# Optimization experiments

Hardware: AMD Instinct MI355X
Metric: run time of the kernel (lower is better)

## Reference

```python
import jax, jax.numpy as jnp
import numpy as np

N_NODES = 100000
N_EDGES = 1600000
IN_DIM = 64
HID = 128
N_GRAPHS = 64
N_CLASSES = 2
EPS = 1e-5


def setup_inputs() -> dict:
    key = jax.random.key(0)
    ks = jax.random.split(key, 8)
    x = jax.random.normal(ks[0], (N_NODES, IN_DIM), dtype=jnp.float32)
    edge_index = jax.random.randint(ks[1], (2, N_EDGES), 0, N_NODES, dtype=jnp.int64)
    batch = jnp.sort(jax.random.randint(ks[2], (N_NODES,), 0, N_GRAPHS, dtype=jnp.int64))
    W1 = jax.random.normal(ks[3], (IN_DIM, HID), dtype=jnp.float32) / np.sqrt(IN_DIM)
    b1 = jnp.zeros((HID,), jnp.float32)
    W2 = jax.random.normal(ks[4], (HID, HID), dtype=jnp.float32) / np.sqrt(HID)
    b2 = jnp.zeros((HID,), jnp.float32)
    gamma = jnp.ones((HID,), jnp.float32)
    beta = jnp.zeros((HID,), jnp.float32)
    fcW = jax.random.normal(ks[5], (HID, N_CLASSES), dtype=jnp.float32) / np.sqrt(HID)
    fcb = jnp.zeros((N_CLASSES,), jnp.float32)
    return {"x": x, "edge_index": edge_index, "batch": batch, "W1": W1, "b1": b1,
            "W2": W2, "b2": b2, "gamma": gamma, "beta": beta, "fcW": fcW, "fcb": fcb}


def reference(x, edge_index, batch, W1, b1, W2, b2, gamma, beta, fcW, fcb):
    n = x.shape[0]
    loop = jnp.arange(n)
    # GCNConv adds self-loops and uses symmetric normalization D^-1/2 (A+I) D^-1/2
    src = jnp.concatenate([edge_index[0], loop])
    dst = jnp.concatenate([edge_index[1], loop])
    deg = jax.ops.segment_sum(jnp.ones_like(dst, dtype=x.dtype), dst, num_segments=n)
    dis = jax.lax.rsqrt(deg)  # deg >= 1 thanks to self-loops
    enorm = dis[src] * dis[dst]  # [E+N]

    def gcn(h, W, b):
        h = h @ W                                   # transform first (PyG order)
        msg = h[src] * enorm[:, None]               # gather + scale
        return jax.ops.segment_sum(msg, dst, num_segments=n) + b  # scatter-add

    cnt = jnp.maximum(jax.ops.segment_sum(jnp.ones((n,), x.dtype), batch,
                                          num_segments=N_GRAPHS), 1.0)[:, None]

    def inst_norm(h):
        # per-graph, per-channel normalization over nodes (affine=False)
        mean = jax.ops.segment_sum(h, batch, num_segments=N_GRAPHS) / cnt
        var = jax.ops.segment_sum(h * h, batch, num_segments=N_GRAPHS) / cnt - mean * mean
        return (h - mean[batch]) * jax.lax.rsqrt(var[batch] + EPS)

    h = jax.nn.relu(inst_norm(gcn(x, W1, b1)))   # dropout = identity (eval)
    h = jax.nn.relu(inst_norm(gcn(h, W2, b2)))
    pooled = jax.ops.segment_sum(h, batch, num_segments=N_GRAPHS) / cnt  # global mean pool
    # BatchNorm1d over the graph dimension (batch statistics, affine)
    m = jnp.mean(pooled, axis=0)
    v = jnp.mean((pooled - m) ** 2, axis=0)
    z = (pooled - m) * jax.lax.rsqrt(v + EPS) * gamma + beta
    return z @ fcW + fcb
```

## Files before the change

kernel.cpp:

```cpp
#include <hip/hip_runtime.h>
#include <hip/hip_bf16.h>


#define HID 128
#define NGRAPH 64
#define EPSN 1e-5f
#define BSHIFT 8
#define NBMAX 512
#define REP 4
#define NH (NGRAPH * HID)

typedef unsigned int uint;
typedef unsigned short ushort;
typedef __attribute__((ext_vector_type(8))) short short8;
typedef __attribute__((ext_vector_type(4))) float f32x4;

static __device__ __forceinline__ ushort f2bf(float f) {
  uint x = __float_as_uint(f);
  return (ushort)((x + 0x7FFFu + ((x >> 16) & 1u)) >> 16);
}
static __device__ __forceinline__ uint pack2(float a, float b) {
  return (uint)f2bf(a) | ((uint)f2bf(b) << 16);
}
static __device__ __forceinline__ float bf_lo(uint u) { return __uint_as_float(u << 16); }
static __device__ __forceinline__ float bf_hi(uint u) {
  return __uint_as_float(u & 0xFFFF0000u);
}

__global__ __launch_bounds__(256) void graph_starts(const int* __restrict__ batch,
                                                    int* __restrict__ gstart, int N) {
  int i = blockIdx.x * 256 + threadIdx.x;
  if (i >= N) return;
  int g = batch[i];
  if (i == 0) {
    for (int q = 0; q <= g; ++q) gstart[q] = 0;
  } else {
    int gp = batch[i - 1];
    if (g != gp)
      for (int q = gp + 1; q <= g; ++q) gstart[q] = i;
  }
  if (i == N - 1)
    for (int q = g + 1; q <= NGRAPH; ++q) gstart[q] = N;
}

__global__ __launch_bounds__(256) void bin_edges(const int* __restrict__ src,
                                                 const int* __restrict__ dst,
                                                 int* __restrict__ gcursor,
                                                 uint* __restrict__ records, int E, int NB,
                                                 int cap) {
  __shared__ int h[NBMAX];
  __shared__ int base[NBMAX];
  for (int i = threadIdx.x; i < NB; i += 256) h[i] = 0;
  __syncthreads();
  int e0 = blockIdx.x * 4096;
  int d[16], s[16];
#pragma unroll
  for (int k = 0; k < 16; ++k) {
    int e = e0 + k * 256 + threadIdx.x;
    if (e < E) {
      d[k] = dst[e];
      s[k] = src[e];
      atomicAdd(&h[d[k] >> BSHIFT], 1);
    }
  }
  __syncthreads();
  for (int i = threadIdx.x; i < NB; i += 256) {
    int c = h[i];
    if (c) base[i] = i * cap + atomicAdd(&gcursor[i], c);
  }
  __syncthreads();
  for (int i = threadIdx.x; i < NB; i += 256) h[i] = 0;
  __syncthreads();
#pragma unroll
  for (int k = 0; k < 16; ++k) {
    int e = e0 + k * 256 + threadIdx.x;
    if (e < E) {
      int b = d[k] >> BSHIFT;
      int lp = atomicAdd(&h[b], 1);
      records[base[b] + lp] = ((uint)s[k] << 8) | (uint)(d[k] & 255);
    }
  }
}

__global__ __launch_bounds__(256) void build_csr(const uint* __restrict__ records,
                                                 const int* __restrict__ gcursor,
                                                 int* __restrict__ row_beg,
                                                 int* __restrict__ row_end,
                                                 float* __restrict__ dis,
                                                 int* __restrict__ esrc, int N, int cap) {
  const int b = blockIdx.x;
  const int node0 = b << BSHIFT;
  const int nn = min(256, N - node0);
  const int beg = b * cap;
  const int cnt = gcursor[b];
  const int t = threadIdx.x;
  __shared__ int lc[256], sc[256], lcur[256];
  lc[t] = 0;
  __syncthreads();
  for (int i = t; i < cnt; i += 256) atomicAdd(&lc[records[beg + i] & 255u], 1);
  __syncthreads();
  int myc = lc[t];
  sc[t] = myc;
  __syncthreads();
  for (int off = 1; off < 256; off <<= 1) {
    int add = (t >= off) ? sc[t - off] : 0;
    __syncthreads();
    sc[t] += add;
    __syncthreads();
  }
  int excl = sc[t] - myc;
  if (t < nn) {
    row_beg[node0 + t] = beg + excl;
    row_end[node0 + t] = beg + excl + myc;
    dis[node0 + t] = rsqrtf((float)myc + 1.0f);
  }
  lcur[t] = excl;
  __syncthreads();
  for (int i = t; i < cnt; i += 256) {
    uint r = records[beg + i];
    int p = atomicAdd(&lcur[r & 255u], 1);
    esrc[beg + p] = (int)(r >> 8);
  }
}

__global__ __launch_bounds__(256) void xscale_bf16(const float* __restrict__ X,
                                                   const float* __restrict__ dis,
                                                   ushort* __restrict__ XS, int n4) {
  int i4 = blockIdx.x * 256 + threadIdx.x;
  if (i4 >= n4) return;
  int n = i4 >> 4;
  float dn = dis[n];
  float4 v = ((const float4*)X)[i4];
  ushort4 u;
  u.x = f2bf(v.x * dn);
  u.y = f2bf(v.y * dn);
  u.z = f2bf(v.z * dn);
  u.w = f2bf(v.w * dn);
  ((ushort4*)XS)[i4] = u;
}

__global__ __launch_bounds__(256) void wt_both(const float* __restrict__ W1,
                                               const float* __restrict__ W2,
                                               ushort* __restrict__ w1t,
                                               ushort* __restrict__ w2t) {
  int i = blockIdx.x * 256 + threadIdx.x;
  if (i < 128 * 64) {
    int c = i / 64, k = i - c * 64;
    w1t[i] = f2bf(W1[(size_t)k * HID + c]);
  } else {
    int i2 = i - 128 * 64;
    if (i2 < 128 * 128) {
      int c = i2 / 128, k = i2 - c * 128;
      w2t[i2] = f2bf(W2[(size_t)k * HID + c]);
    }
  }
}

__global__ __launch_bounds__(256) void aggregate64(const ushort* __restrict__ XS,
                                                   const int* __restrict__ row_beg,
                                                   const int* __restrict__ row_end,
                                                   const int* __restrict__ esrc,
                                                   const float* __restrict__ dis,
                                                   ushort* __restrict__ out, int N) {
  int wave = (int)((blockIdx.x * 256 + threadIdx.x) >> 6);
  const int l = threadIdx.x & 63;
  const int n = wave * 4 + (l >> 4);
  if (n >= N) return;
  const int j = l & 15;
  const float dn = dis[n];
  const int beg = row_beg[n];
  const int len = row_end[n] - beg;
  const uint2* Xj = (const uint2*)XS + j;
  float a0 = 0.f, a1 = 0.f, a2 = 0.f, a3 = 0.f;
  float b0 = 0.f, b1 = 0.f, b2 = 0.f, b3 = 0.f;
  int i = 0;
  for (; i + 7 < len; i += 8) {
    int s0 = esrc[beg + i], s1 = esrc[beg + i + 1];
    int s2 = esrc[beg + i + 2], s3 = esrc[beg + i + 3];
    int s4 = esrc[beg + i + 4], s5 = esrc[beg + i + 5];
    int s6 = esrc[beg + i + 6], s7 = esrc[beg + i + 7];
    uint2 u0 = Xj[(size_t)s0 * 16];
    uint2 u1 = Xj[(size_t)s1 * 16];
    uint2 u2 = Xj[(size_t)s2 * 16];
    uint2 u3 = Xj[(size_t)s3 * 16];
    uint2 u4 = Xj[(size_t)s4 * 16];
    uint2 u5 = Xj[(size_t)s5 * 16];
    uint2 u6 = Xj[(size_t)s6 * 16];
    uint2 u7 = Xj[(size_t)s7 * 16];
    a0 += bf_lo(u0.x) + bf_lo(u1.x) + bf_lo(u2.x) + bf_lo(u3.x);
    a1 += bf_hi(u0.x) + bf_hi(u1.x) + bf_hi(u2.x) + bf_hi(u3.x);
    a2 += bf_lo(u0.y) + bf_lo(u1.y) + bf_lo(u2.y) + bf_lo(u3.y);
    a3 += bf_hi(u0.y) + bf_hi(u1.y) + bf_hi(u2.y) + bf_hi(u3.y);
    b0 += bf_lo(u4.x) + bf_lo(u5.x) + bf_lo(u6.x) + bf_lo(u7.x);
    b1 += bf_hi(u4.x) + bf_hi(u5.x) + bf_hi(u6.x) + bf_hi(u7.x);
    b2 += bf_lo(u4.y) + bf_lo(u5.y) + bf_lo(u6.y) + bf_lo(u7.y);
    b3 += bf_hi(u4.y) + bf_hi(u5.y) + bf_hi(u6.y) + bf_hi(u7.y);
  }
  for (; i < len; ++i) {
    uint2 u = Xj[(size_t)esrc[beg + i] * 16];
    a0 += bf_lo(u.x);
    a1 += bf_hi(u.x);
    a2 += bf_lo(u.y);
    a3 += bf_hi(u.y);
  }
  uint2 us = Xj[(size_t)n * 16];
  a0 += b0 + bf_lo(us.x);
  a1 += b1 + bf_hi(us.x);
  a2 += b2 + bf_lo(us.y);
  a3 += b3 + bf_hi(us.y);
  uint2 o;
  o.x = pack2(a0 * dn, a1 * dn);
  o.y = pack2(a2 * dn, a3 * dn);
  ((uint2*)out)[(size_t)n * 16 + j] = o;
}

__global__ __launch_bounds__(256) void aggregate128(const ushort* __restrict__ H,
                                                    const int* __restrict__ row_beg,
                                                    const int* __restrict__ row_end,
                                                    const int* __restrict__ esrc,
                                                    const float* __restrict__ dis,
                                                    const float* __restrict__ bias,
                                                    ushort* __restrict__ outz, int N) {
  int wave = (int)((blockIdx.x * 256 + threadIdx.x) >> 6);
  const int l = threadIdx.x & 63;
  const int n = wave * 4 + (l >> 4);
  if (n >= N) return;
  const int j = l & 15;
  const float dn = dis[n];
  const int beg = row_beg[n];
  const int len = row_end[n] - beg;
  const uint4* Hj = (const uint4*)H + j;
  float a0 = 0.f, a1 = 0.f, a2 = 0.f, a3 = 0.f;
  float a4 = 0.f, a5 = 0.f, a6 = 0.f, a7 = 0.f;
  float b0 = 0.f, b1 = 0.f, b2 = 0.f, b3 = 0.f;
  float b4 = 0.f, b5 = 0.f, b6 = 0.f, b7 = 0.f;
  int i = 0;
  for (; i + 7 < len; i += 8) {
    int s0 = esrc[beg + i], s1 = esrc[beg + i + 1];
    int s2 = esrc[beg + i + 2], s3 = esrc[beg + i + 3];
    int s4 = esrc[beg + i + 4], s5 = esrc[beg + i + 5];
    int s6 = esrc[beg + i + 6], s7 = esrc[beg + i + 7];
    uint4 u0 = Hj[(size_t)s0 * 16];
    uint4 u1 = Hj[(size_t)s1 * 16];
    uint4 u2 = Hj[(size_t)s2 * 16];
    uint4 u3 = Hj[(size_t)s3 * 16];
    uint4 u4 = Hj[(size_t)s4 * 16];
    uint4 u5 = Hj[(size_t)s5 * 16];
    uint4 u6 = Hj[(size_t)s6 * 16];
    uint4 u7 = Hj[(size_t)s7 * 16];
    a0 += bf_lo(u0.x) + bf_lo(u1.x) + bf_lo(u2.x) + bf_lo(u3.x);
    a1 += bf_hi(u0.x) + bf_hi(u1.x) + bf_hi(u2.x) + bf_hi(u3.x);
    a2 += bf_lo(u0.y) + bf_lo(u1.y) + bf_lo(u2.y) + bf_lo(u3.y);
    a3 += bf_hi(u0.y) + bf_hi(u1.y) + bf_hi(u2.y) + bf_hi(u3.y);
    a4 += bf_lo(u0.z) + bf_lo(u1.z) + bf_lo(u2.z) + bf_lo(u3.z);
    a5 += bf_hi(u0.z) + bf_hi(u1.z) + bf_hi(u2.z) + bf_hi(u3.z);
    a6 += bf_lo(u0.w) + bf_lo(u1.w) + bf_lo(u2.w) + bf_lo(u3.w);
    a7 += bf_hi(u0.w) + bf_hi(u1.w) + bf_hi(u2.w) + bf_hi(u3.w);
    b0 += bf_lo(u4.x) + bf_lo(u5.x) + bf_lo(u6.x) + bf_lo(u7.x);
    b1 += bf_hi(u4.x) + bf_hi(u5.x) + bf_hi(u6.x) + bf_hi(u7.x);
    b2 += bf_lo(u4.y) + bf_lo(u5.y) + bf_lo(u6.y) + bf_lo(u7.y);
    b3 += bf_hi(u4.y) + bf_hi(u5.y) + bf_hi(u6.y) + bf_hi(u7.y);
    b4 += bf_lo(u4.z) + bf_lo(u5.z) + bf_lo(u6.z) + bf_lo(u7.z);
    b5 += bf_hi(u4.z) + bf_hi(u5.z) + bf_hi(u6.z) + bf_hi(u7.z);
    b6 += bf_lo(u4.w) + bf_lo(u5.w) + bf_lo(u6.w) + bf_lo(u7.w);
    b7 += bf_hi(u4.w) + bf_hi(u5.w) + bf_hi(u6.w) + bf_hi(u7.w);
  }
  for (; i < len; ++i) {
    uint4 u = Hj[(size_t)esrc[beg + i] * 16];
    a0 += bf_lo(u.x);
    a1 += bf_hi(u.x);
    a2 += bf_lo(u.y);
    a3 += bf_hi(u.y);
    a4 += bf_lo(u.z);
    a5 += bf_hi(u.z);
    a6 += bf_lo(u.w);
    a7 += bf_hi(u.w);
  }
  uint4 us = Hj[(size_t)n * 16];
  a0 += b0 + bf_lo(us.x);
  a1 += b1 + bf_hi(us.x);
  a2 += b2 + bf_lo(us.y);
  a3 += b3 + bf_hi(us.y);
  a4 += b4 + bf_lo(us.z);
  a5 += b5 + bf_hi(us.z);
  a6 += b6 + bf_lo(us.w);
  a7 += b7 + bf_hi(us.w);
  float4 bv0 = ((const float4*)bias)[2 * j];
  float4 bv1 = ((const float4*)bias)[2 * j + 1];
  uint4 o;
  o.x = pack2(a0 * dn + bv0.x, a1 * dn + bv0.y);
  o.y = pack2(a2 * dn + bv0.z, a3 * dn + bv0.w);
  o.z = pack2(a4 * dn + bv1.x, a5 * dn + bv1.y);
  o.w = pack2(a6 * dn + bv1.z, a7 * dn + bv1.w);
  ((uint4*)outz)[(size_t)n * 16 + j] = o;
}

template <int K, bool FUSE_NORM, bool DIS_SCALE, bool HAS_BIAS>
__global__ __launch_bounds__(256) void gemm_mfma(const ushort* __restrict__ X,
                                                 const ushort* __restrict__ Wt,
                                                 const float* __restrict__ bias,
                                                 const int* __restrict__ batch,
                                                 const float* __restrict__ mean,
                                                 const float* __restrict__ inv,
                                                 const float* __restrict__ disv,
                                                 ushort* __restrict__ Y, int N) {
  const int t = threadIdx.x;
  const int w = t >> 6;
  const int l = t & 63;
  const int lr = l & 15;
  const int lk = l >> 4;
  const int row0 = blockIdx.x * 64 + w * 16;
  const int arow = min(row0 + lr, N - 1);
  int g = 0;
  if (FUSE_NORM) g = batch[arow];
  f32x4 acc[8];
#pragma unroll
  for (int i = 0; i < 8; ++i) acc[i] = (f32x4){0.f, 0.f, 0.f, 0.f};
#pragma unroll
  for (int k0 = 0; k0 < K; k0 += 32) {
    const int kbase = k0 + lk * 8;
    short8 a = *(const short8*)(X + (size_t)arow * K + kbase);
    if (FUSE_NORM) {
      const float* mp = mean + g * HID + kbase;
      const float* ip = inv + g * HID + kbase;
      short8 an;
#pragma unroll
      for (int j = 0; j < 8; ++j) {
        float f = __uint_as_float((uint)(ushort)a[j] << 16);
        f = fmaxf((f - mp[j]) * ip[j], 0.f);
        an[j] = (short)f2bf(f);
      }
      a = an;
    }
#pragma unroll
    for (int nf = 0; nf < 8; ++nf) {
      short8 b = *(const short8*)(Wt + (size_t)(nf * 16 + lr) * K + kbase);
      acc[nf] = __builtin_amdgcn_mfma_f32_16x16x32_bf16(a, b, acc[nf], 0, 0, 0);
    }
  }
#pragma unroll
  for (int r = 0; r < 4; ++r) {
    int grow = row0 + lk * 4 + r;
    if (grow < N) {
      float ds = DIS_SCALE ? disv[grow] : 1.f;
#pragma unroll
      for (int nf = 0; nf < 8; ++nf) {
        int col = nf * 16 + lr;
        float v = acc[nf][r];
        if (HAS_BIAS) v += bias[col];
        v *= ds;
        Y[(size_t)grow * HID + col] = f2bf(v);
      }
    }
  }
}

__global__ __launch_bounds__(256) void stats_pass(const ushort* __restrict__ G,
                                                  const int* __restrict__ batch,
                                                  float* __restrict__ gsum,
                                                  float* __restrict__ gsq, int N) {
  const int c2 = threadIdx.x & 63;
  const int sub = threadIdx.x >> 6;
  const int n0 = blockIdx.x * 64 + sub * 16;
  const int n1 = min(n0 + 16, N);
  const int roff = (blockIdx.x & (REP - 1)) * NH;
  float* gs = gsum + roff;
  float* gq = gsq + roff;
  const uint* Gj = (const uint*)G + c2;
  float s0 = 0.f, s1 = 0.f, q0 = 0.f, q1 = 0.f;
  int cur = -1;
  for (int n = n0; n < n1; ++n) {
    int g = batch[n];
    if (g != cur) {
      if (cur >= 0) {
        atomicAdd(&gs[cur * HID + 2 * c2], s0);
        atomicAdd(&gs[cur * HID + 2 * c2 + 1], s1);
        atomicAdd(&gq[cur * HID + 2 * c2], q0);
        atomicAdd(&gq[cur * HID + 2 * c2 + 1], q1);
      }
      cur = g;
      s0 = s1 = q0 = q1 = 0.f;
    }
    uint u = Gj[(size_t)n * 64];
    float v0 = bf_lo(u), v1 = bf_hi(u);
    s0 += v0;
    s1 += v1;
    q0 += v0 * v0;
    q1 += v1 * v1;
  }
  if (cur >= 0) {
    atomicAdd(&gs[cur * HID + 2 * c2], s0);
    atomicAdd(&gs[cur * HID + 2 * c2 + 1], s1);
    atomicAdd(&gq[cur * HID + 2 * c2], q0);
    atomicAdd(&gq[cur * HID + 2 * c2 + 1], q1);
  }
}

__global__ __launch_bounds__(256) void finalize_stats(const float* __restrict__ gsum,
                                                      const float* __restrict__ gsq,
                                                      const int* __restrict__ gstart,
                                                      float* __restrict__ mean,
                                                      float* __restrict__ inv) {
  int i = blockIdx.x * 256 + threadIdx.x;
  if (i >= NH) return;
  int g = i >> 7;
  float c = fmaxf((float)(gstart[g + 1] - gstart[g]), 1.f);
  float s = gsum[i] + gsum[i + NH] + gsum[i + 2 * NH] + gsum[i + 3 * NH];
  float q = gsq[i] + gsq[i + NH] + gsq[i + 2 * NH] + gsq[i + 3 * NH];
  float m = s / c;
  float v = q / c - m * m;
  mean[i] = m;
  inv[i] = rsqrtf(v + EPSN);
}

__global__ __launch_bounds__(256) void norm_relu_pool(const ushort* __restrict__ G,
                                                      const int* __restrict__ batch,
                                                      const float* __restrict__ mean,
                                                      const float* __restrict__ inv,
                                                      float* __restrict__ pooled, int N) {
  const int c2 = threadIdx.x & 63;
  const int sub = threadIdx.x >> 6;
  const int n0 = blockIdx.x * 64 + sub * 16;
  const int n1 = min(n0 + 16, N);
  float* pl = pooled + (blockIdx.x & (REP - 1)) * NH;
  const uint* Gj = (const uint*)G + c2;
  float p0 = 0.f, p1 = 0.f;
  int cur = -1;
  float2 mv = {0.f, 0.f}, iv = {0.f, 0.f};
  for (int n = n0; n < n1; ++n) {
    int g = batch[n];
    if (g != cur) {
      if (cur >= 0) {
        atomicAdd(&pl[cur * HID + 2 * c2], p0);
        atomicAdd(&pl[cur * HID + 2 * c2 + 1], p1);
      }
      cur = g;
      p0 = p1 = 0.f;
      mv = ((const float2*)mean)[g * 64 + c2];
      iv = ((const float2*)inv)[g * 64 + c2];
    }
    uint u = Gj[(size_t)n * 64];
    p0 += fmaxf((bf_lo(u) - mv.x) * iv.x, 0.f);
    p1 += fmaxf((bf_hi(u) - mv.y) * iv.y, 0.f);
  }
  if (cur >= 0) {
    atomicAdd(&pl[cur * HID + 2 * c2], p0);
    atomicAdd(&pl[cur * HID + 2 * c2 + 1], p1);
  }
}

__global__ __launch_bounds__(256) void final_head(const float* __restrict__ pooled_sum,
                                                  const int* __restrict__ gstart,
                                                  const float* __restrict__ gamma,
                                                  const float* __restrict__ beta,
                                                  const float* __restrict__ fcW,
                                                  const float* __restrict__ fcb,
                                                  float* __restrict__ out) {
  __shared__ float P[NGRAPH][HID];
  __shared__ float zs[HID], zb[HID];
  int t = threadIdx.x;
  for (int i = t; i < NH; i += 256) {
    int g = i >> 7;
    float c = fmaxf((float)(gstart[g + 1] - gstart[g]), 1.f);
    float s = pooled_sum[i] + pooled_sum[i + NH] + pooled_sum[i + 2 * NH] +
              pooled_sum[i + 3 * NH];
    P[g][i & 127] = s / c;
  }
  __syncthreads();
  if (t < HID) {
    float m = 0.f;
    for (int g = 0; g < NGRAPH; ++g) m += P[g][t];
    m *= (1.f / NGRAPH);
    float v = 0.f;
    for (int g = 0; g < NGRAPH; ++g) {
      float d = P[g][t] - m;
      v += d * d;
    }
    v *= (1.f / NGRAPH);
    float sc = rsqrtf(v + EPSN) * gamma[t];
    zs[t] = sc;
    zb[t] = beta[t] - m * sc;
  }
  __syncthreads();
  if (t < NGRAPH * 2) {
    int g = t >> 1, k = t & 1;
    float acc = fcb[k];
    for (int c = 0; c < HID; ++c) {
      float z = P[g][c] * zs[c] + zb[c];
      acc += z * fcW[c * 2 + k];
    }
    out[t] = acc;
  }
}

extern "C" void kernel_launch(void* const* d_in, const int* in_sizes, int n_in,
                              void* d_out, int out_size, void* d_ws, size_t ws_size,
                              hipStream_t stream) {
  const float* x = (const float*)d_in[0];
  const int* ei = (const int*)d_in[1];
  const int* batch = (const int*)d_in[2];
  const float* W1 = (const float*)d_in[3];
  const float* b1 = (const float*)d_in[4];
  const float* W2 = (const float*)d_in[5];
  const float* b2 = (const float*)d_in[6];
  const float* gamma = (const float*)d_in[7];
  const float* beta = (const float*)d_in[8];
  const float* fcW = (const float*)d_in[9];
  const float* fcb = (const float*)d_in[10];
  float* out = (float*)d_out;

  const int N = in_sizes[2];
  const int E = in_sizes[1] / 2;
  const int* srcp = ei;
  const int* dstp = ei + E;
  const int NB = (N + 255) >> BSHIFT;
  const int cap = 2 * (E / NB) + 256;

  float* ws = (float*)d_ws;
  size_t off = 0;
  auto alloc = [&](size_t n) {
    float* p = ws + off;
    off += (n + 127) & ~(size_t)127;
    return p;
  };
  int* row_beg = (int*)alloc(N);
  int* row_end = (int*)alloc(N);
  int* esrc = (int*)alloc((size_t)NB * cap);
  size_t recsz = ((size_t)NB * cap > (size_t)N * 32 ? (size_t)NB * cap : (size_t)N * 32);
  float* recbuf = alloc(recsz);
  float* dis = alloc(N);
  float* y1b = alloc((size_t)N * 32);
  float* h1b = alloc((size_t)N * 64);
  float* h2b = alloc((size_t)N * 64);
  float* zb_ = alloc((size_t)N * 64);
  float* w1tb = alloc(128 * 64 / 2);
  float* w2tb = alloc(128 * 128 / 2);
  int* gstart = (int*)alloc(NGRAPH + 1);
  float* zero0 = ws + off;
  int* gcursor = (int*)alloc(NBMAX);
  float* gsum1 = alloc(NH * REP);
  float* gsq1 = alloc(NH * REP);
  float* gsum2 = alloc(NH * REP);
  float* gsq2 = alloc(NH * REP);
  float* pooled = alloc(NH * REP);
  size_t zero_bytes = (size_t)((ws + off) - zero0) * sizeof(float);
  float* mean1 = alloc(NH);
  float* inv1 = alloc(NH);
  float* mean2 = alloc(NH);
  float* inv2 = alloc(NH);

  uint* records = (uint*)recbuf;
  ushort* xs = (ushort*)recbuf;
  ushort* y1 = (ushort*)y1b;
  ushort* h1 = (ushort*)h1b;
  ushort* h2s = (ushort*)h2b;
  ushort* z = (ushort*)zb_;
  ushort* w1t = (ushort*)w1tb;
  ushort* w2t = (ushort*)w2tb;

  const int nblkN = (N + 255) / 256;
  const int nblkE4k = (E + 4095) / 4096;

  hipMemsetAsync(zero0, 0, zero_bytes, stream);

  wt_both<<<(128 * 64 + 128 * 128 + 255) / 256, 256, 0, stream>>>(W1, W2, w1t, w2t);
  graph_starts<<<nblkN, 256, 0, stream>>>(batch, gstart, N);
  bin_edges<<<nblkE4k, 256, 0, stream>>>(srcp, dstp, gcursor, records, E, NB, cap);
  build_csr<<<NB, 256, 0, stream>>>(records, gcursor, row_beg, row_end, dis, esrc, N, cap);

  const int aggBlocks = ((N + 3) / 4 + 3) / 4;
  const int gemmBlocks = (N + 63) / 64;
  const int nrmBlocks = (N + 63) / 64;

  xscale_bf16<<<(N * 16 + 255) / 256, 256, 0, stream>>>(x, dis, xs, N * 16);
  aggregate64<<<aggBlocks, 256, 0, stream>>>(xs, row_beg, row_end, esrc, dis, y1, N);
  gemm_mfma<64, false, false, true><<<gemmBlocks, 256, 0, stream>>>(
      y1, w1t, b1, nullptr, nullptr, nullptr, nullptr, h1, N);
  stats_pass<<<nrmBlocks, 256, 0, stream>>>(h1, batch, gsum1, gsq1, N);
  finalize_stats<<<(NH + 255) / 256, 256, 0, stream>>>(gsum1, gsq1, gstart, mean1, inv1);

  gemm_mfma<128, true, true, false><<<gemmBlocks, 256, 0, stream>>>(
      h1, w2t, nullptr, batch, mean1, inv1, dis, h2s, N);
  aggregate128<<<aggBlocks, 256, 0, stream>>>(h2s, row_beg, row_end, esrc, dis, b2, z, N);
  stats_pass<<<nrmBlocks, 256, 0, stream>>>(z, batch, gsum2, gsq2, N);
  finalize_stats<<<(NH + 255) / 256, 256, 0, stream>>>(gsum2, gsq2, gstart, mean2, inv2);
  norm_relu_pool<<<nrmBlocks, 256, 0, stream>>>(z, batch, mean2, inv2, pooled, N);

  final_head<<<1, 256, 0, stream>>>(pooled, gstart, gamma, beta, fcW, fcb, out);
}
```

Measured before the change: 295.5 us.

## Fuse per-graph instance-norm statistics into GEMM and aggregation epilogues

The separate stats_pass kernels are removed. Per-graph sum and sum-of-squares are now accumulated in the epilogue of the first GEMM and of aggregate128, using wave shuffles when a group of rows belongs to one graph and per-element atomics otherwise. This saves two kernel launches and two full re-reads of the N×128 bf16 activations. In exchange, the number of atomics rises: the fast path in aggregate128 still issues 16 atomics per lane for every 4 nodes, versus the old per-16-node accumulation, so atomic contention may grow.

```diff
diff --git a/kernel.cpp b/kernel.cpp
--- a/kernel.cpp
+++ b/kernel.cpp
@@ -220,6 +220,9 @@
                                                     const int* __restrict__ esrc,
                                                     const float* __restrict__ dis,
                                                     const float* __restrict__ bias,
+                                                    const int* __restrict__ batch,
+                                                    float* __restrict__ gsum,
+                                                    float* __restrict__ gsq,
                                                     ushort* __restrict__ outz, int N) {
   int wave = (int)((blockIdx.x * 256 + threadIdx.x) >> 6);
   const int l = threadIdx.x & 63;
@@ -293,9 +296,45 @@
   o.z = pack2(a4 * dn + bv1.x, a5 * dn + bv1.y);
   o.w = pack2(a6 * dn + bv1.z, a7 * dn + bv1.w);
   ((uint4*)outz)[(size_t)n * 16 + j] = o;
-}
-
-template <int K, bool FUSE_NORM, bool DIS_SCALE, bool HAS_BIAS>
+
+  float s[8], q[8];
+  s[0] = bf_lo(o.x); s[1] = bf_hi(o.x); s[2] = bf_lo(o.y); s[3] = bf_hi(o.y);
+  s[4] = bf_lo(o.z); s[5] = bf_hi(o.z); s[6] = bf_lo(o.w); s[7] = bf_hi(o.w);
+#pragma unroll
+  for (int k = 0; k < 8; ++k) q[k] = s[k] * s[k];
+  const int roff = (wave & (REP - 1)) * NH;
+  const bool fast = (wave * 4 + 3 < N) && (batch[wave * 4] == batch[wave * 4 + 3]);
+  if (fast) {
+#pragma unroll
+    for (int k = 0; k < 8; ++k) {
+      s[k] += __shfl_xor(s[k], 16, 64);
+      q[k] += __shfl_xor(q[k], 16, 64);
+      s[k] += __shfl_xor(s[k], 32, 64);
+      q[k] += __shfl_xor(q[k], 32, 64);
+    }
+    if ((l >> 4) == 0) {
+      int g = batch[wave * 4];
+      float* gs = gsum + roff + g * HID + 8 * j;
+      float* gq = gsq + roff + g * HID + 8 * j;
+#pragma unroll
+      for (int k = 0; k < 8; ++k) {
+        atomicAdd(gs + k, s[k]);
+        atomicAdd(gq + k, q[k]);
+      }
+    }
+  } else {
+    int g = batch[n];
+    float* gs = gsum + roff + g * HID + 8 * j;
+    float* gq = gsq + roff + g * HID + 8 * j;
+#pragma unroll
+    for (int k = 0; k < 8; ++k) {
+      atomicAdd(gs + k, s[k]);
+      atomicAdd(gq + k, q[k]);
+    }
+  }
+}
+
+template <int K, bool FUSE_NORM, bool DIS_SCALE, bool HAS_BIAS, bool STATS>
 __global__ __launch_bounds__(256) void gemm_mfma(const ushort* __restrict__ X,
                                                  const ushort* __restrict__ Wt,
                                                  const float* __restrict__ bias,
@@ -303,6 +342,8 @@
                                                  const float* __restrict__ mean,
                                                  const float* __restrict__ inv,
                                                  const float* __restrict__ disv,
+                                                 float* __restrict__ gsum,
+                                                 float* __restrict__ gsq,
                                                  ushort* __restrict__ Y, int N) {
   const int t = threadIdx.x;
   const int w = t >> 6;
@@ -338,6 +379,13 @@
       acc[nf] = __builtin_amdgcn_mfma_f32_16x16x32_bf16(a, b, acc[nf], 0, 0, 0);
     }
   }
+  const bool fast = STATS && (row0 + 15 < N) && (batch[row0] == batch[row0 + 15]);
+  const int roff = STATS ? ((blockIdx.x & (REP - 1)) * NH) : 0;
+  float s8[8], q8[8];
+  if (STATS) {
+#pragma unroll
+    for (int i = 0; i < 8; ++i) s8[i] = q8[i] = 0.f;
+  }
 #pragma unroll
   for (int r = 0; r < 4; ++r) {
     int grow = row0 + lk * 4 + r;
@@ -349,50 +397,40 @@
         float v = acc[nf][r];
         if (HAS_BIAS) v += bias[col];
         v *= ds;
-        Y[(size_t)grow * HID + col] = f2bf(v);
+        ushort hv = f2bf(v);
+        Y[(size_t)grow * HID + col] = hv;
+        if (STATS) {
+          float fr = __uint_as_float((uint)hv << 16);
+          if (fast) {
+            s8[nf] += fr;
+            q8[nf] += fr * fr;
+          } else {
+            int gg = batch[grow];
+            atomicAdd(&gsum[roff + gg * HID + col], fr);
+            atomicAdd(&gsq[roff + gg * HID + col], fr * fr);
+          }
+        }
       }
     }
   }
-}
-
-__global__ __launch_bounds__(256) void stats_pass(const ushort* __restrict__ G,
-                                                  const int* __restrict__ batch,
-                                                  float* __restrict__ gsum,
-                                                  float* __restrict__ gsq, int N) {
-  const int c2 = threadIdx.x & 63;
-  const int sub = threadIdx.x >> 6;
-  const int n0 = blockIdx.x * 64 + sub * 16;
-  const int n1 = min(n0 + 16, N);
-  const int roff = (blockIdx.x & (REP - 1)) * NH;
-  float* gs = gsum + roff;
-  float* gq = gsq + roff;
-  const uint* Gj = (const uint*)G + c2;
-  float s0 = 0.f, s1 = 0.f, q0 = 0.f, q1 = 0.f;
-  int cur = -1;
-  for (int n = n0; n < n1; ++n) {
-    int g = batch[n];
-    if (g != cur) {
-      if (cur >= 0) {
-        atomicAdd(&gs[cur * HID + 2 * c2], s0);
-        atomicAdd(&gs[cur * HID + 2 * c2 + 1], s1);
-        atomicAdd(&gq[cur * HID + 2 * c2], q0);
-        atomicAdd(&gq[cur * HID + 2 * c2 + 1], q1);
+  if (STATS && fast) {
+#pragma unroll
+    for (int i = 0; i < 8; ++i) {
+      s8[i] += __shfl_xor(s8[i], 16, 64);
+      q8[i] += __shfl_xor(q8[i], 16, 64);
+      s8[i] += __shfl_xor(s8[i], 32, 64);
+      q8[i] += __shfl_xor(q8[i], 32, 64);
+    }
+    if (lk == 0) {
+      int gg = batch[row0];
+      float* gs = gsum + roff + gg * HID;
+      float* gq = gsq + roff + gg * HID;
+#pragma unroll
+      for (int nf = 0; nf < 8; ++nf) {
+        atomicAdd(&gs[nf * 16 + lr], s8[nf]);
+        atomicAdd(&gq[nf * 16 + lr], q8[nf]);
       }
-      cur = g;
-      s0 = s1 = q0 = q1 = 0.f;
-    }
-    uint u = Gj[(size_t)n * 64];
-    float v0 = bf_lo(u), v1 = bf_hi(u);
-    s0 += v0;
-    s1 += v1;
-    q0 += v0 * v0;
-    q1 += v1 * v1;
-  }
-  if (cur >= 0) {
-    atomicAdd(&gs[cur * HID + 2 * c2], s0);
-    atomicAdd(&gs[cur * HID + 2 * c2 + 1], s1);
-    atomicAdd(&gq[cur * HID + 2 * c2], q0);
-    atomicAdd(&gq[cur * HID + 2 * c2 + 1], q1);
+    }
   }
 }
 
@@ -574,15 +612,14 @@
 
   xscale_bf16<<<(N * 16 + 255) / 256, 256, 0, stream>>>(x, dis, xs, N * 16);
   aggregate64<<<aggBlocks, 256, 0, stream>>>(xs, row_beg, row_end, esrc, dis, y1, N);
-  gemm_mfma<64, false, false, true><<<gemmBlocks, 256, 0, stream>>>(
-      y1, w1t, b1, nullptr, nullptr, nullptr, nullptr, h1, N);
-  stats_pass<<<nrmBlocks, 256, 0, stream>>>(h1, batch, gsum1, gsq1, N);
+  gemm_mfma<64, false, false, true, true><<<gemmBlocks, 256, 0, stream>>>(
+      y1, w1t, b1, batch, nullptr, nullptr, nullptr, gsum1, gsq1, h1, N);
   finalize_stats<<<(NH + 255) / 256, 256, 0, stream>>>(gsum1, gsq1, gstart, mean1, inv1);
 
-  gemm_mfma<128, true, true, false><<<gemmBlocks, 256, 0, stream>>>(
-      h1, w2t, nullptr, batch, mean1, inv1, dis, h2s, N);
-  aggregate128<<<aggBlocks, 256, 0, stream>>>(h2s, row_beg, row_end, esrc, dis, b2, z, N);
-  stats_pass<<<nrmBlocks, 256, 0, stream>>>(z, batch, gsum2, gsq2, N);
+  gemm_mfma<128, true, true, false, false><<<gemmBlocks, 256, 0, stream>>>(
+      h1, w2t, nullptr, batch, mean1, inv1, dis, nullptr, nullptr, h2s, N);
+  aggregate128<<<aggBlocks, 256, 0, stream>>>(h2s, row_beg, row_end, esrc, dis, b2, batch,
+                                              gsum2, gsq2, z, N);
   finalize_stats<<<(NH + 255) / 256, 256, 0, stream>>>(gsum2, gsq2, gstart, mean2, inv2);
   norm_relu_pool<<<nrmBlocks, 256, 0, stream>>>(z, batch, mean2, inv2, pooled, N);
 
```

Result: slower. 764.2 us (+158.6%).
